# Optimization experiments

Measured on AMD Instinct MI355X. Metric: run time of the kernel, lower is better.

Reference implementation:

```python
import jax, jax.numpy as jnp
import numpy as np

EMBED_DIM = 768
N_HEADS = 12
HEAD_DIM = EMBED_DIM // N_HEADS


def setup_inputs() -> dict:
    key = jax.random.key(0)
    ks = jax.random.split(key, 6)
    bsz, seq = 2, 4096
    hidden_states = jax.random.normal(ks[0], (bsz, seq, EMBED_DIM), dtype=jnp.float32)
    attention_mask = jnp.zeros((bsz, 1, 1, seq), dtype=jnp.float32)
    s = 1.0 / np.sqrt(EMBED_DIM)
    Wq = jax.random.normal(ks[1], (EMBED_DIM, EMBED_DIM), dtype=jnp.float32) * s
    Wk = jax.random.normal(ks[2], (EMBED_DIM, EMBED_DIM), dtype=jnp.float32) * s
    Wv = jax.random.normal(ks[3], (EMBED_DIM, EMBED_DIM), dtype=jnp.float32) * s
    Wo = jax.random.normal(ks[4], (EMBED_DIM, EMBED_DIM), dtype=jnp.float32) * s
    bo = jax.random.normal(ks[5], (EMBED_DIM,), dtype=jnp.float32) * s
    return {"hidden_states": hidden_states, "attention_mask": attention_mask,
            "Wq": Wq, "Wk": Wk, "Wv": Wv, "Wo": Wo, "bo": bo}


def reference(hidden_states, attention_mask, Wq, Wk, Wv, Wo, bo):
    bsz, seq, _ = hidden_states.shape
    scale = 1.0 / np.sqrt(HEAD_DIM)

    def split_heads(x):  # [b, s, e] -> [b, h, s, d]
        return x.reshape(bsz, seq, N_HEADS, HEAD_DIM).transpose(0, 2, 1, 3)

    # nn.Linear applies x @ W.T
    q = split_heads(hidden_states @ Wq.T)
    k = split_heads(hidden_states @ Wk.T)
    v = split_heads(hidden_states @ Wv.T)

    # [b, h, tgt, src] score matrix (faithful to the bmm+softmax+bmm original)
    attn = jnp.einsum('bhqd,bhkd->bhqk', q, k) * scale
    attn = attn + attention_mask  # mask broadcasts [b,1,1,src]
    probs = jax.nn.softmax(attn, axis=-1)
    ctx = jnp.einsum('bhqk,bhkd->bhqd', probs, v)

    concat = ctx.transpose(0, 2, 1, 3).reshape(bsz, seq, EMBED_DIM)
    return concat @ Wo.T + bo
```

## Files before the change

kernel.cpp:

```cpp
#include <hip/hip_runtime.h>
#include <stdint.h>

#define ED   768
#define NH   12
#define HD   64
#define SEQ  4096
#define BSZ  2
#define BHT  (BSZ*NH)
#define MTOT (BSZ*SEQ)

typedef short bf16x8  __attribute__((ext_vector_type(8)));
typedef float f32x4   __attribute__((ext_vector_type(4)));
typedef float f32x16  __attribute__((ext_vector_type(16)));
typedef unsigned int u32x4 __attribute__((ext_vector_type(4)));

#define LOG2E 1.44269504088896340736f
#define C2    (0.125f * LOG2E)

__device__ __forceinline__ unsigned short f2bf(float f) {
    union { float f; uint32_t u; } v; v.f = f;
    uint32_t u = v.u;
    u += 0x7fffu + ((u >> 16) & 1u);
    return (unsigned short)(u >> 16);
}

__device__ __forceinline__ uint32_t cvtpk(float lo, float hi) {
    uint32_t r;
    asm("v_cvt_pk_bf16_f32 %0, %1, %2" : "=v"(r) : "v"(lo), "v"(hi));
    return r;
}

__device__ __forceinline__ void cp16(const unsigned short* g, unsigned short* l) {
    __builtin_amdgcn_global_load_lds(
        (const __attribute__((address_space(1))) unsigned int*)(const void*)g,
        (__attribute__((address_space(3))) unsigned int*)(void*)l,
        16, 0, 0);
}

#define H_CHUNKS  (MTOT * ED / 4)
#define W_CHUNKS  (ED * ED / 4)
#define CVT_TOTAL (H_CHUNKS + 4 * W_CHUNKS)

__global__ __launch_bounds__(256) void convert_bf16(
    const float* __restrict__ H,  const float* __restrict__ Wq,
    const float* __restrict__ Wk, const float* __restrict__ Wv,
    const float* __restrict__ Wo, unsigned short* __restrict__ dst,
    unsigned short* __restrict__ WoB) {
    int i4 = blockIdx.x * 256 + threadIdx.x;
    float4 v;
    ushort4* optr;
    if (i4 < H_CHUNKS) { v = ((const float4*)H)[i4]; optr = (ushort4*)dst + i4; }
    else {
        int j = i4 - H_CHUNKS;
        if (j < 3 * W_CHUNKS) {
            if (j < W_CHUNKS)          v = ((const float4*)Wq)[j];
            else if (j < 2 * W_CHUNKS) v = ((const float4*)Wk)[j - W_CHUNKS];
            else                       v = ((const float4*)Wv)[j - 2 * W_CHUNKS];
            optr = (ushort4*)dst + i4;
        } else {
            v = ((const float4*)Wo)[j - 3 * W_CHUNKS];
            optr = (ushort4*)WoB + (j - 3 * W_CHUNKS);
        }
    }
    ushort4 o;
    o.x = f2bf(v.x); o.y = f2bf(v.y); o.z = f2bf(v.z); o.w = f2bf(v.w);
    *optr = o;
}

__global__ __launch_bounds__(256) void qkv_gemm(
    const unsigned short* __restrict__ Hb,
    const unsigned short* __restrict__ Wb,
    unsigned short* __restrict__ qkv) {
    __shared__ __align__(16) unsigned short Ah[128 * 64];
    __shared__ __align__(16) unsigned short Bh[128 * 64];
    const int t = threadIdx.x, w = t >> 6, lane = t & 63;
    const int quad = lane >> 4, r16 = lane & 15;
    const int wm = w >> 1, wn = w & 1;
    const int m0 = blockIdx.y * 128, n0g = blockIdx.x * 128;
    const int wsel = n0g / ED, n0 = n0g % ED;
    const int lrow = lane >> 3;
    const int lchs = ((lane & 7) ^ (lrow & 7)) * 8;

    f32x4 acc[4][4] = {};
    for (int kt = 0; kt < ED / 64; ++kt) {
        const int k0 = kt * 64;
#pragma unroll
        for (int i = 0; i < 4; ++i) {
            int row = i * 32 + w * 8;
            cp16(&Hb[(size_t)(m0 + row + lrow) * ED + k0 + lchs], &Ah[row * 64]);
            cp16(&Wb[(size_t)(n0g + row + lrow) * ED + k0 + lchs], &Bh[row * 64]);
        }
        __syncthreads();
#pragma unroll
        for (int kk = 0; kk < 2; ++kk) {
            bf16x8 aF[4], bF[4];
#pragma unroll
            for (int mi = 0; mi < 4; ++mi) {
                int R = wm * 64 + mi * 16 + r16;
                aF[mi] = *(const bf16x8*)&Ah[R * 64 + (((kk * 4 + quad) ^ (r16 & 7)) * 8)];
            }
#pragma unroll
            for (int ni = 0; ni < 4; ++ni) {
                int R = wn * 64 + ni * 16 + r16;
                bF[ni] = *(const bf16x8*)&Bh[R * 64 + (((kk * 4 + quad) ^ (r16 & 7)) * 8)];
            }
            if (wsel == 2) {
#pragma unroll
                for (int mi = 0; mi < 4; ++mi)
#pragma unroll
                    for (int ni = 0; ni < 4; ++ni)
                        acc[mi][ni] = __builtin_amdgcn_mfma_f32_16x16x32_bf16(
                            bF[ni], aF[mi], acc[mi][ni], 0, 0, 0);
            } else {
#pragma unroll
                for (int mi = 0; mi < 4; ++mi)
#pragma unroll
                    for (int ni = 0; ni < 4; ++ni)
                        acc[mi][ni] = __builtin_amdgcn_mfma_f32_16x16x32_bf16(
                            aF[mi], bF[ni], acc[mi][ni], 0, 0, 0);
            }
        }
        __syncthreads();
    }
    const size_t WSZ = (size_t)BHT * SEQ * HD;
    if (wsel == 2) {
#pragma unroll
        for (int mi = 0; mi < 4; ++mi)
#pragma unroll
            for (int ni = 0; ni < 4; ++ni)
#pragma unroll
                for (int r = 0; r < 4; ++r) {
                    int m  = m0 + wm * 64 + mi * 16 + r16;
                    int nn = n0 + wn * 64 + ni * 16 + quad * 4 + r;
                    int b = m >> 12, s = m & 4095;
                    int hh = nn >> 6, dd = nn & 63;
                    qkv[2 * WSZ + (((size_t)b * NH + hh) * HD + dd) * SEQ + s] =
                        f2bf(acc[mi][ni][r]);
                }
    } else {
        const float sc = (wsel == 0) ? C2 : 1.0f;
#pragma unroll
        for (int mi = 0; mi < 4; ++mi)
#pragma unroll
            for (int ni = 0; ni < 4; ++ni)
#pragma unroll
                for (int r = 0; r < 4; ++r) {
                    int m = m0 + wm * 64 + mi * 16 + quad * 4 + r;
                    int b = m >> 12, s = m & 4095;
                    int nn = n0 + wn * 64 + ni * 16 + r16;
                    int hh = nn >> 6, dd = nn & 63;
                    size_t off = (((size_t)b * NH + hh) * SEQ + s) * HD + dd;
                    qkv[(size_t)wsel * WSZ + off] = f2bf(acc[mi][ni][r] * sc);
                }
    }
}

__global__ __launch_bounds__(256) void flash_attn(
    const unsigned short* __restrict__ qkv, const float* __restrict__ mask,
    unsigned short* __restrict__ ctx) {
    __shared__ __align__(16) unsigned short Ksm[2][64 * 64];
    __shared__ __align__(16) unsigned short Vtsm[2][64 * 64];
    __shared__ __align__(16) unsigned short Mall[SEQ];
    const int t  = threadIdx.x;
    const int bh = blockIdx.y;
    const int b  = bh / NH;
    const int h  = bh % NH;
    const int qbase = blockIdx.x * 128;
    const size_t WSZ = (size_t)BHT * SEQ * HD;
    const unsigned short* Qp = qkv + (size_t)bh * SEQ * HD;
    const unsigned short* Kp = Qp + WSZ;
    const unsigned short* Vt = qkv + 2 * WSZ + (size_t)bh * HD * SEQ;
    const int w = t >> 6, lane = t & 63, n31 = lane & 31, hi = lane >> 5;
    const int lrow = lane >> 3;
    const int lchs = ((lane & 7) ^ (lrow & 7)) * 8;

    bf16x8 qF[4];
    {
        int qrow = qbase + w * 32 + n31;
#pragma unroll
        for (int kc = 0; kc < 4; ++kc)
            qF[kc] = *(const bf16x8*)&Qp[(size_t)qrow * HD + kc * 16 + hi * 8];
    }
    bf16x8 bOnes = {};
    if (hi == 0) bOnes[0] = (short)0x3F80;
    bf16x8 aOnes;
#pragma unroll
    for (int i = 0; i < 8; ++i) aOnes[i] = (short)0x3F80;

#pragma unroll
    for (int i = 0; i < 4; ++i) {
        float4 mv = ((const float4*)(mask + (size_t)b * SEQ))[i * 256 + t];
        ushort4 o;
        o.x = f2bf(LOG2E * mv.x); o.y = f2bf(LOG2E * mv.y);
        o.z = f2bf(LOG2E * mv.z); o.w = f2bf(LOG2E * mv.w);
        *(ushort4*)&Mall[(i * 256 + t) * 4] = o;
    }

#pragma unroll
    for (int i = 0; i < 2; ++i) {
        int row = w * 16 + i * 8;
        cp16(&Kp[(size_t)(row + lrow) * HD + lchs], &Ksm[0][row * 64]);
        cp16(&Vt[(size_t)(row + lrow) * SEQ + lchs], &Vtsm[0][row * 64]);
    }
    __syncthreads();

    f32x16 oAcc[2] = {};
    f32x16 lAcc = {};
    const int sw = n31 & 7;
    int cur = 0;

    for (int kt = 0; kt < SEQ / 64; ++kt) {
        if (kt + 1 < SEQ / 64) {
#pragma unroll
            for (int i = 0; i < 2; ++i) {
                int row = w * 16 + i * 8;
                cp16(&Kp[(size_t)((kt + 1) * 64 + row + lrow) * HD + lchs],
                     &Ksm[cur ^ 1][row * 64]);
                cp16(&Vt[(size_t)(row + lrow) * SEQ + (kt + 1) * 64 + lchs],
                     &Vtsm[cur ^ 1][row * 64]);
            }
        }

        float p[2][16];
#pragma unroll
        for (int st = 0; st < 2; ++st) {
            bf16x8 am = {};
            {
                unsigned short mv = Mall[kt * 64 + st * 32 + n31];
                am[0] = (hi == 0) ? (short)mv : (short)0;
            }
            f32x16 sA = {};
            sA = __builtin_amdgcn_mfma_f32_32x32x16_bf16(am, bOnes, sA, 0, 0, 0);
            __builtin_amdgcn_s_setprio(1);
#pragma unroll
            for (int kc = 0; kc < 4; ++kc) {
                bf16x8 kF = *(const bf16x8*)
                    &Ksm[cur][(st * 32 + n31) * 64 + (((2 * kc + hi) ^ sw) * 8)];
                sA = __builtin_amdgcn_mfma_f32_32x32x16_bf16(kF, qF[kc], sA, 0, 0, 0);
            }
            __builtin_amdgcn_s_setprio(0);
#pragma unroll
            for (int r = 0; r < 16; ++r) p[st][r] = __builtin_amdgcn_exp2f(sA[r]);
        }

        bf16x8 pF[4];
#pragma unroll
        for (int st = 0; st < 2; ++st) {
            uint32_t pw[8];
#pragma unroll
            for (int i = 0; i < 8; ++i)
                pw[i] = cvtpk(p[st][2 * i], p[st][2 * i + 1]);
#pragma unroll
            for (int half = 0; half < 2; ++half) {
                auto r02 = __builtin_amdgcn_permlane32_swap(
                    pw[half * 4 + 0], pw[half * 4 + 2], false, false);
                auto r13 = __builtin_amdgcn_permlane32_swap(
                    pw[half * 4 + 1], pw[half * 4 + 3], false, false);
                union { u32x4 u; bf16x8 h; } f;
                f.u[0] = r02[0]; f.u[1] = r13[0]; f.u[2] = r02[1]; f.u[3] = r13[1];
                pF[st * 2 + half] = f.h;
            }
        }

        __builtin_amdgcn_s_setprio(1);
#pragma unroll
        for (int kc = 0; kc < 4; ++kc) {
            lAcc = __builtin_amdgcn_mfma_f32_32x32x16_bf16(
                aOnes, pF[kc], lAcc, 0, 0, 0);
#pragma unroll
            for (int dt = 0; dt < 2; ++dt) {
                bf16x8 vF = *(const bf16x8*)
                    &Vtsm[cur][(dt * 32 + n31) * 64 + (((2 * kc + hi) ^ sw) * 8)];
                oAcc[dt] = __builtin_amdgcn_mfma_f32_32x32x16_bf16(vF, pF[kc], oAcc[dt], 0, 0, 0);
            }
        }
        __builtin_amdgcn_s_setprio(0);

        __syncthreads();
        cur ^= 1;
    }
    float inv = 1.0f / lAcc[0];
    int s = qbase + w * 32 + n31;
    unsigned short* obase = &ctx[((size_t)b * SEQ + s) * ED + h * HD];
#pragma unroll
    for (int dt = 0; dt < 2; ++dt)
#pragma unroll
        for (int g = 0; g < 4; ++g) {
            ushort4 o;
            o.x = f2bf(oAcc[dt][4 * g + 0] * inv);
            o.y = f2bf(oAcc[dt][4 * g + 1] * inv);
            o.z = f2bf(oAcc[dt][4 * g + 2] * inv);
            o.w = f2bf(oAcc[dt][4 * g + 3] * inv);
            *(ushort4*)&obase[dt * 32 + hi * 4 + 8 * g] = o;
        }
}

__global__ __launch_bounds__(256) void out_gemm(
    const unsigned short* __restrict__ Ab,
    const unsigned short* __restrict__ Wob,
    const float* __restrict__ bo, float* __restrict__ out) {
    __shared__ __align__(16) unsigned short Ah[128 * 64];
    __shared__ __align__(16) unsigned short Bh[128 * 64];
    const int t = threadIdx.x, w = t >> 6, lane = t & 63;
    const int quad = lane >> 4, r16 = lane & 15;
    const int wm = w >> 1, wn = w & 1;
    const int m0 = blockIdx.y * 128, n0 = blockIdx.x * 128;
    const int lrow = lane >> 3;
    const int lchs = ((lane & 7) ^ (lrow & 7)) * 8;

    f32x4 acc[4][4] = {};
    for (int kt = 0; kt < ED / 64; ++kt) {
        const int k0 = kt * 64;
#pragma unroll
        for (int i = 0; i < 4; ++i) {
            int row = i * 32 + w * 8;
            cp16(&Ab[(size_t)(m0 + row + lrow) * ED + k0 + lchs], &Ah[row * 64]);
            cp16(&Wob[(size_t)(n0 + row + lrow) * ED + k0 + lchs], &Bh[row * 64]);
        }
        __syncthreads();
#pragma unroll
        for (int kk = 0; kk < 2; ++kk) {
            bf16x8 aF[4], bF[4];
#pragma unroll
            for (int mi = 0; mi < 4; ++mi) {
                int R = wm * 64 + mi * 16 + r16;
                aF[mi] = *(const bf16x8*)&Ah[R * 64 + (((kk * 4 + quad) ^ (r16 & 7)) * 8)];
            }
#pragma unroll
            for (int ni = 0; ni < 4; ++ni) {
                int R = wn * 64 + ni * 16 + r16;
                bF[ni] = *(const bf16x8*)&Bh[R * 64 + (((kk * 4 + quad) ^ (r16 & 7)) * 8)];
            }
#pragma unroll
            for (int mi = 0; mi < 4; ++mi)
#pragma unroll
                for (int ni = 0; ni < 4; ++ni)
                    acc[mi][ni] = __builtin_amdgcn_mfma_f32_16x16x32_bf16(
                        aF[mi], bF[ni], acc[mi][ni], 0, 0, 0);
        }
        __syncthreads();
    }
    float bov[4];
#pragma unroll
    for (int ni = 0; ni < 4; ++ni) bov[ni] = bo[n0 + wn * 64 + ni * 16 + r16];
#pragma unroll
    for (int mi = 0; mi < 4; ++mi)
#pragma unroll
        for (int ni = 0; ni < 4; ++ni)
#pragma unroll
            for (int r = 0; r < 4; ++r) {
                int m = m0 + wm * 64 + mi * 16 + quad * 4 + r;
                int n = n0 + wn * 64 + ni * 16 + r16;
                out[(size_t)m * ED + n] = acc[mi][ni][r] + bov[ni];
            }
}

extern "C" void kernel_launch(void* const* d_in, const int* in_sizes, int n_in,
                              void* d_out, int out_size, void* d_ws, size_t ws_size,
                              hipStream_t stream) {
    const float* H    = (const float*)d_in[0];
    const float* mask = (const float*)d_in[1];
    const float* Wq   = (const float*)d_in[2];
    const float* Wk   = (const float*)d_in[3];
    const float* Wv   = (const float*)d_in[4];
    const float* Wo   = (const float*)d_in[5];
    const float* bo   = (const float*)d_in[6];
    unsigned short* ws = (unsigned short*)d_ws;
    const size_t WSZ = (size_t)BHT * SEQ * HD;
    unsigned short* qkv = ws;
    unsigned short* ctx = ws + 3 * WSZ;
    unsigned short* WoB = ctx + (size_t)MTOT * ED;
    float* out = (float*)d_out;
    unsigned short* Hb = (unsigned short*)d_out;
    unsigned short* Wb = Hb + (size_t)MTOT * ED;

    convert_bf16<<<CVT_TOTAL / 256, 256, 0, stream>>>(H, Wq, Wk, Wv, Wo, Hb, WoB);
    qkv_gemm<<<dim3(3 * ED / 128, MTOT / 128), 256, 0, stream>>>(Hb, Wb, qkv);
    flash_attn<<<dim3(SEQ / 128, BHT), 256, 0, stream>>>(qkv, mask, ctx);
    out_gemm<<<dim3(ED / 128, MTOT / 128), 256, 0, stream>>>(ctx, WoB, bo, out);
}
```

Before: 295.1 us.

## Split flash attention over key range into two halves with combine kernel

Templates the attention kernel on a key-range split. With SPLIT=2 each block processes half the keys and writes unnormalized fp32 partial outputs and row sums. A new kernel then adds the halves, normalizes and converts to bf16. The intent is to double the available parallelism and shorten each block's serial loop. The cost is extra fp32 global traffic and an additional launch. The split path is used only when the workspace is large enough.

```diff
diff --git a/kernel.cpp b/kernel.cpp
--- a/kernel.cpp
+++ b/kernel.cpp
@@ -22,6 +22,11 @@
     uint32_t u = v.u;
     u += 0x7fffu + ((u >> 16) & 1u);
     return (unsigned short)(u >> 16);
+}
+
+__device__ __forceinline__ float bf2f(unsigned short h) {
+    union { uint32_t u; float f; } v; v.u = ((uint32_t)h) << 16;
+    return v.f;
 }
 
 __device__ __forceinline__ uint32_t cvtpk(float lo, float hi) {
@@ -155,21 +160,26 @@
     }
 }
 
+template <int SPLIT>
 __global__ __launch_bounds__(256) void flash_attn(
     const unsigned short* __restrict__ qkv, const float* __restrict__ mask,
-    unsigned short* __restrict__ ctx) {
+    unsigned short* __restrict__ ctx, float* __restrict__ Ap0,
+    float* __restrict__ Ap1, float* __restrict__ lp) {
+    constexpr int KRANGE = SEQ / SPLIT;
+    constexpr int NT = KRANGE / 64;
     __shared__ __align__(16) unsigned short Ksm[2][64 * 64];
     __shared__ __align__(16) unsigned short Vtsm[2][64 * 64];
-    __shared__ __align__(16) unsigned short Mall[SEQ];
+    __shared__ __align__(16) unsigned short Mall[KRANGE];
     const int t  = threadIdx.x;
     const int bh = blockIdx.y;
     const int b  = bh / NH;
     const int h  = bh % NH;
+    const int half = (SPLIT == 2) ? blockIdx.z : 0;
     const int qbase = blockIdx.x * 128;
     const size_t WSZ = (size_t)BHT * SEQ * HD;
     const unsigned short* Qp = qkv + (size_t)bh * SEQ * HD;
-    const unsigned short* Kp = Qp + WSZ;
-    const unsigned short* Vt = qkv + 2 * WSZ + (size_t)bh * HD * SEQ;
+    const unsigned short* Kp = Qp + WSZ + (size_t)half * KRANGE * HD;
+    const unsigned short* Vt = qkv + 2 * WSZ + (size_t)bh * HD * SEQ + (size_t)half * KRANGE;
     const int w = t >> 6, lane = t & 63, n31 = lane & 31, hi = lane >> 5;
     const int lrow = lane >> 3;
     const int lchs = ((lane & 7) ^ (lrow & 7)) * 8;
@@ -188,8 +198,8 @@
     for (int i = 0; i < 8; ++i) aOnes[i] = (short)0x3F80;
 
 #pragma unroll
-    for (int i = 0; i < 4; ++i) {
-        float4 mv = ((const float4*)(mask + (size_t)b * SEQ))[i * 256 + t];
+    for (int i = 0; i < KRANGE / 1024; ++i) {
+        float4 mv = ((const float4*)(mask + (size_t)b * SEQ + half * KRANGE))[i * 256 + t];
         ushort4 o;
         o.x = f2bf(LOG2E * mv.x); o.y = f2bf(LOG2E * mv.y);
         o.z = f2bf(LOG2E * mv.z); o.w = f2bf(LOG2E * mv.w);
@@ -209,8 +219,8 @@
     const int sw = n31 & 7;
     int cur = 0;
 
-    for (int kt = 0; kt < SEQ / 64; ++kt) {
-        if (kt + 1 < SEQ / 64) {
+    for (int kt = 0; kt < NT; ++kt) {
+        if (kt + 1 < NT) {
 #pragma unroll
             for (int i = 0; i < 2; ++i) {
                 int row = w * 16 + i * 8;
@@ -251,14 +261,14 @@
             for (int i = 0; i < 8; ++i)
                 pw[i] = cvtpk(p[st][2 * i], p[st][2 * i + 1]);
 #pragma unroll
-            for (int half = 0; half < 2; ++half) {
+            for (int half2 = 0; half2 < 2; ++half2) {
                 auto r02 = __builtin_amdgcn_permlane32_swap(
-                    pw[half * 4 + 0], pw[half * 4 + 2], false, false);
+                    pw[half2 * 4 + 0], pw[half2 * 4 + 2], false, false);
                 auto r13 = __builtin_amdgcn_permlane32_swap(
-                    pw[half * 4 + 1], pw[half * 4 + 3], false, false);
+                    pw[half2 * 4 + 1], pw[half2 * 4 + 3], false, false);
                 union { u32x4 u; bf16x8 h; } f;
                 f.u[0] = r02[0]; f.u[1] = r13[0]; f.u[2] = r02[1]; f.u[3] = r13[1];
-                pF[st * 2 + half] = f.h;
+                pF[st * 2 + half2] = f.h;
             }
         }
 
@@ -279,20 +289,62 @@
         __syncthreads();
         cur ^= 1;
     }
-    float inv = 1.0f / lAcc[0];
+
     int s = qbase + w * 32 + n31;
-    unsigned short* obase = &ctx[((size_t)b * SEQ + s) * ED + h * HD];
-#pragma unroll
-    for (int dt = 0; dt < 2; ++dt)
-#pragma unroll
-        for (int g = 0; g < 4; ++g) {
-            ushort4 o;
-            o.x = f2bf(oAcc[dt][4 * g + 0] * inv);
-            o.y = f2bf(oAcc[dt][4 * g + 1] * inv);
-            o.z = f2bf(oAcc[dt][4 * g + 2] * inv);
-            o.w = f2bf(oAcc[dt][4 * g + 3] * inv);
-            *(ushort4*)&obase[dt * 32 + hi * 4 + 8 * g] = o;
-        }
+    if (SPLIT == 1) {
+        float inv = 1.0f / lAcc[0];
+        unsigned short* obase = &ctx[((size_t)b * SEQ + s) * ED + h * HD];
+#pragma unroll
+        for (int dt = 0; dt < 2; ++dt)
+#pragma unroll
+            for (int g = 0; g < 4; ++g) {
+                ushort4 o;
+                o.x = f2bf(oAcc[dt][4 * g + 0] * inv);
+                o.y = f2bf(oAcc[dt][4 * g + 1] * inv);
+                o.z = f2bf(oAcc[dt][4 * g + 2] * inv);
+                o.w = f2bf(oAcc[dt][4 * g + 3] * inv);
+                *(ushort4*)&obase[dt * 32 + hi * 4 + 8 * g] = o;
+            }
+    } else {
+        float* Ap = half ? Ap1 : Ap0;
+        float* obase = &Ap[((size_t)b * SEQ + s) * ED + h * HD];
+#pragma unroll
+        for (int dt = 0; dt < 2; ++dt)
+#pragma unroll
+            for (int g = 0; g < 4; ++g) {
+                float4 o;
+                o.x = oAcc[dt][4 * g + 0];
+                o.y = oAcc[dt][4 * g + 1];
+                o.z = oAcc[dt][4 * g + 2];
+                o.w = oAcc[dt][4 * g + 3];
+                *(float4*)&obase[dt * 32 + hi * 4 + 8 * g] = o;
+            }
+        if (hi == 0)
+            lp[(size_t)half * BHT * SEQ + (size_t)bh * SEQ + s] = lAcc[0];
+    }
+}
+
+__global__ __launch_bounds__(256) void combine_halves(
+    const float* __restrict__ A0, const float* __restrict__ A1,
+    const float* __restrict__ lp, unsigned short* __restrict__ ctx) {
+    int i8 = blockIdx.x * 256 + threadIdx.x;
+    int e0 = i8 * 8;
+    int m = e0 / ED;
+    int e = e0 - m * ED;
+    int b = m >> 12, s = m & 4095, h = e >> 6;
+    size_t bhs = ((size_t)(b * NH + h)) * SEQ + s;
+    float inv = 1.0f / (lp[bhs] + lp[(size_t)BHT * SEQ + bhs]);
+    float4 a0 = ((const float4*)A0)[i8 * 2];
+    float4 a1 = ((const float4*)A1)[i8 * 2];
+    float4 b0 = ((const float4*)A0)[i8 * 2 + 1];
+    float4 b1 = ((const float4*)A1)[i8 * 2 + 1];
+    ushort4 o0, o1;
+    o0.x = f2bf((a0.x + a1.x) * inv); o0.y = f2bf((a0.y + a1.y) * inv);
+    o0.z = f2bf((a0.z + a1.z) * inv); o0.w = f2bf((a0.w + a1.w) * inv);
+    o1.x = f2bf((b0.x + b1.x) * inv); o1.y = f2bf((b0.y + b1.y) * inv);
+    o1.z = f2bf((b0.z + b1.z) * inv); o1.w = f2bf((b0.w + b1.w) * inv);
+    ((ushort4*)ctx)[i8 * 2]     = o0;
+    ((ushort4*)ctx)[i8 * 2 + 1] = o1;
 }
 
 __global__ __launch_bounds__(256) void out_gemm(
@@ -373,9 +425,21 @@
     float* out = (float*)d_out;
     unsigned short* Hb = (unsigned short*)d_out;
     unsigned short* Wb = Hb + (size_t)MTOT * ED;
+    float* lpart = (float*)(WoB + (size_t)ED * ED);
+    float* A1    = lpart + 2 * (size_t)BHT * SEQ;
+    float* A0    = (float*)d_out;
+    const size_t need = ((size_t)(3 * WSZ + (size_t)MTOT * ED + ED * ED)) * 2
+                      + 2 * (size_t)BHT * SEQ * 4 + (size_t)MTOT * ED * 4;
 
     convert_bf16<<<CVT_TOTAL / 256, 256, 0, stream>>>(H, Wq, Wk, Wv, Wo, Hb, WoB);
     qkv_gemm<<<dim3(3 * ED / 128, MTOT / 128), 256, 0, stream>>>(Hb, Wb, qkv);
-    flash_attn<<<dim3(SEQ / 128, BHT), 256, 0, stream>>>(qkv, mask, ctx);
+    if (ws_size >= need) {
+        flash_attn<2><<<dim3(SEQ / 128, BHT, 2), 256, 0, stream>>>(
+            qkv, mask, ctx, A0, A1, lpart);
+        combine_halves<<<(MTOT * ED / 8) / 256, 256, 0, stream>>>(A0, A1, lpart, ctx);
+    } else {
+        flash_attn<1><<<dim3(SEQ / 128, BHT), 256, 0, stream>>>(
+            qkv, mask, ctx, nullptr, nullptr, nullptr);
+    }
     out_gemm<<<dim3(ED / 128, MTOT / 128), 256, 0, stream>>>(ctx, WoB, bo, out);
 }
```

After: 316.3 us. 1.07x slower.

## Triple-buffer K tiles and split barriers with partial vmcnt waits in flash attention

Applied to the files above, without the earlier changes.

Restructures the flash-attention main loop so K tiles are prefetched two iterations ahead into a three-slot LDS ring while V stays double-buffered. The single end-of-iteration __syncthreads is replaced by an s_waitcnt vmcnt(N) plus s_barrier placed before the PV stage and a bare barrier after it, and the last two iterations are peeled out. The aim is to give global-to-LDS loads more time to land and to stop the barrier from draining all outstanding loads. In exchange it uses more LDS, which can lower occupancy, and it relies on exact hand-counted vmcnt values to be correct.

```diff
diff --git a/kernel.cpp b/kernel.cpp
--- a/kernel.cpp
+++ b/kernel.cpp
@@ -155,11 +155,67 @@
     }
 }
 
+#define QK_SM(KOFF, KT, PF) do {                                               \
+    float p_[2][16];                                                           \
+_Pragma("unroll")                                                              \
+    for (int st = 0; st < 2; ++st) {                                           \
+        bf16x8 am = {};                                                        \
+        { unsigned short mv = Mall[(KT) * 64 + st * 32 + n31];                 \
+          am[0] = (hi == 0) ? (short)mv : (short)0; }                          \
+        f32x16 sA = {};                                                        \
+        sA = __builtin_amdgcn_mfma_f32_32x32x16_bf16(am, bOnes, sA, 0, 0, 0);  \
+        __builtin_amdgcn_s_setprio(1);                                         \
+_Pragma("unroll")                                                              \
+        for (int kc = 0; kc < 4; ++kc) {                                       \
+            bf16x8 kF = *(const bf16x8*)                                       \
+                &Ksm[(KOFF) + (st * 32 + n31) * 64 + (((2 * kc + hi) ^ sw) * 8)]; \
+            sA = __builtin_amdgcn_mfma_f32_32x32x16_bf16(kF, qF[kc], sA, 0, 0, 0); \
+        }                                                                      \
+        __builtin_amdgcn_s_setprio(0);                                         \
+_Pragma("unroll")                                                              \
+        for (int r = 0; r < 16; ++r) p_[st][r] = __builtin_amdgcn_exp2f(sA[r]); \
+    }                                                                          \
+_Pragma("unroll")                                                              \
+    for (int st = 0; st < 2; ++st) {                                           \
+        uint32_t pw[8];                                                        \
+_Pragma("unroll")                                                              \
+        for (int i = 0; i < 8; ++i)                                            \
+            pw[i] = cvtpk(p_[st][2 * i], p_[st][2 * i + 1]);                   \
+_Pragma("unroll")                                                              \
+        for (int hf = 0; hf < 2; ++hf) {                                       \
+            auto r02 = __builtin_amdgcn_permlane32_swap(                       \
+                pw[hf * 4 + 0], pw[hf * 4 + 2], false, false);                 \
+            auto r13 = __builtin_amdgcn_permlane32_swap(                       \
+                pw[hf * 4 + 1], pw[hf * 4 + 3], false, false);                 \
+            union { u32x4 u; bf16x8 h; } f_;                                   \
+            f_.u[0] = r02[0]; f_.u[1] = r13[0]; f_.u[2] = r02[1]; f_.u[3] = r13[1]; \
+            PF[st * 2 + hf] = f_.h;                                            \
+        }                                                                      \
+    }                                                                          \
+} while (0)
+
+#define PV_ACC(VOFF, PF) do {                                                  \
+    __builtin_amdgcn_s_setprio(1);                                             \
+_Pragma("unroll")                                                              \
+    for (int kc = 0; kc < 4; ++kc) {                                           \
+        lAcc = __builtin_amdgcn_mfma_f32_32x32x16_bf16(                        \
+            aOnes, PF[kc], lAcc, 0, 0, 0);                                     \
+_Pragma("unroll")                                                              \
+        for (int dt = 0; dt < 2; ++dt) {                                       \
+            bf16x8 vF = *(const bf16x8*)                                       \
+                &Vtsm[(VOFF) + (dt * 32 + n31) * 64 + (((2 * kc + hi) ^ sw) * 8)]; \
+            oAcc[dt] = __builtin_amdgcn_mfma_f32_32x32x16_bf16(                \
+                vF, PF[kc], oAcc[dt], 0, 0, 0);                                \
+        }                                                                      \
+    }                                                                          \
+    __builtin_amdgcn_s_setprio(0);                                             \
+} while (0)
+
 __global__ __launch_bounds__(256) void flash_attn(
     const unsigned short* __restrict__ qkv, const float* __restrict__ mask,
     unsigned short* __restrict__ ctx) {
-    __shared__ __align__(16) unsigned short Ksm[2][64 * 64];
-    __shared__ __align__(16) unsigned short Vtsm[2][64 * 64];
+    __shared__ __align__(16) unsigned short Ksm[3 * 4096];
+    __shared__ __align__(16) unsigned short Vtsm[2 * 4096];
     __shared__ __align__(16) unsigned short Mall[SEQ];
     const int t  = threadIdx.x;
     const int bh = blockIdx.y;
@@ -196,89 +252,55 @@
         *(ushort4*)&Mall[(i * 256 + t) * 4] = o;
     }
 
-#pragma unroll
-    for (int i = 0; i < 2; ++i) {
-        int row = w * 16 + i * 8;
-        cp16(&Kp[(size_t)(row + lrow) * HD + lchs], &Ksm[0][row * 64]);
-        cp16(&Vt[(size_t)(row + lrow) * SEQ + lchs], &Vtsm[0][row * 64]);
-    }
+    const int row0 = w * 16, row1 = w * 16 + 8;
+
+    cp16(&Kp[(size_t)(row0 + lrow) * HD + lchs],      &Ksm[row0 * 64]);
+    cp16(&Kp[(size_t)(row1 + lrow) * HD + lchs],      &Ksm[row1 * 64]);
+    cp16(&Kp[(size_t)(64 + row0 + lrow) * HD + lchs], &Ksm[4096 + row0 * 64]);
+    cp16(&Kp[(size_t)(64 + row1 + lrow) * HD + lchs], &Ksm[4096 + row1 * 64]);
+    cp16(&Vt[(size_t)(row0 + lrow) * SEQ + lchs],     &Vtsm[row0 * 64]);
+    cp16(&Vt[(size_t)(row1 + lrow) * SEQ + lchs],     &Vtsm[row1 * 64]);
     __syncthreads();
 
     f32x16 oAcc[2] = {};
     f32x16 lAcc = {};
     const int sw = n31 & 7;
-    int cur = 0;
-
-    for (int kt = 0; kt < SEQ / 64; ++kt) {
-        if (kt + 1 < SEQ / 64) {
-#pragma unroll
-            for (int i = 0; i < 2; ++i) {
-                int row = w * 16 + i * 8;
-                cp16(&Kp[(size_t)((kt + 1) * 64 + row + lrow) * HD + lchs],
-                     &Ksm[cur ^ 1][row * 64]);
-                cp16(&Vt[(size_t)(row + lrow) * SEQ + (kt + 1) * 64 + lchs],
-                     &Vtsm[cur ^ 1][row * 64]);
-            }
-        }
-
-        float p[2][16];
-#pragma unroll
-        for (int st = 0; st < 2; ++st) {
-            bf16x8 am = {};
-            {
-                unsigned short mv = Mall[kt * 64 + st * 32 + n31];
-                am[0] = (hi == 0) ? (short)mv : (short)0;
-            }
-            f32x16 sA = {};
-            sA = __builtin_amdgcn_mfma_f32_32x32x16_bf16(am, bOnes, sA, 0, 0, 0);
-            __builtin_amdgcn_s_setprio(1);
-#pragma unroll
-            for (int kc = 0; kc < 4; ++kc) {
-                bf16x8 kF = *(const bf16x8*)
-                    &Ksm[cur][(st * 32 + n31) * 64 + (((2 * kc + hi) ^ sw) * 8)];
-                sA = __builtin_amdgcn_mfma_f32_32x32x16_bf16(kF, qF[kc], sA, 0, 0, 0);
-            }
-            __builtin_amdgcn_s_setprio(0);
-#pragma unroll
-            for (int r = 0; r < 16; ++r) p[st][r] = __builtin_amdgcn_exp2f(sA[r]);
-        }
+    int kCur = 0, kNxt = 4096, kFar = 8192;
+    int vCur = 0;
+
+    for (int kt = 0; kt < 62; ++kt) {
+        cp16(&Kp[(size_t)((kt + 2) * 64 + row0 + lrow) * HD + lchs], &Ksm[kFar + row0 * 64]);
+        cp16(&Kp[(size_t)((kt + 2) * 64 + row1 + lrow) * HD + lchs], &Ksm[kFar + row1 * 64]);
+        cp16(&Vt[(size_t)(row0 + lrow) * SEQ + (kt + 1) * 64 + lchs], &Vtsm[(vCur ^ 4096) + row0 * 64]);
+        cp16(&Vt[(size_t)(row1 + lrow) * SEQ + (kt + 1) * 64 + lchs], &Vtsm[(vCur ^ 4096) + row1 * 64]);
 
         bf16x8 pF[4];
-#pragma unroll
-        for (int st = 0; st < 2; ++st) {
-            uint32_t pw[8];
-#pragma unroll
-            for (int i = 0; i < 8; ++i)
-                pw[i] = cvtpk(p[st][2 * i], p[st][2 * i + 1]);
-#pragma unroll
-            for (int half = 0; half < 2; ++half) {
-                auto r02 = __builtin_amdgcn_permlane32_swap(
-                    pw[half * 4 + 0], pw[half * 4 + 2], false, false);
-                auto r13 = __builtin_amdgcn_permlane32_swap(
-                    pw[half * 4 + 1], pw[half * 4 + 3], false, false);
-                union { u32x4 u; bf16x8 h; } f;
-                f.u[0] = r02[0]; f.u[1] = r13[0]; f.u[2] = r02[1]; f.u[3] = r13[1];
-                pF[st * 2 + half] = f.h;
-            }
-        }
-
-        __builtin_amdgcn_s_setprio(1);
-#pragma unroll
-        for (int kc = 0; kc < 4; ++kc) {
-            lAcc = __builtin_amdgcn_mfma_f32_32x32x16_bf16(
-                aOnes, pF[kc], lAcc, 0, 0, 0);
-#pragma unroll
-            for (int dt = 0; dt < 2; ++dt) {
-                bf16x8 vF = *(const bf16x8*)
-                    &Vtsm[cur][(dt * 32 + n31) * 64 + (((2 * kc + hi) ^ sw) * 8)];
-                oAcc[dt] = __builtin_amdgcn_mfma_f32_32x32x16_bf16(vF, pF[kc], oAcc[dt], 0, 0, 0);
-            }
-        }
-        __builtin_amdgcn_s_setprio(0);
-
-        __syncthreads();
-        cur ^= 1;
-    }
+        QK_SM(kCur, kt, pF);
+        asm volatile("s_waitcnt vmcnt(4)\n\ts_barrier" ::: "memory");
+        PV_ACC(vCur, pF);
+        asm volatile("s_barrier" ::: "memory");
+
+        int tmp = kCur; kCur = kNxt; kNxt = kFar; kFar = tmp;
+        vCur ^= 4096;
+    }
+    {
+        cp16(&Vt[(size_t)(row0 + lrow) * SEQ + 63 * 64 + lchs], &Vtsm[(vCur ^ 4096) + row0 * 64]);
+        cp16(&Vt[(size_t)(row1 + lrow) * SEQ + 63 * 64 + lchs], &Vtsm[(vCur ^ 4096) + row1 * 64]);
+        bf16x8 pF[4];
+        QK_SM(kCur, 62, pF);
+        asm volatile("s_waitcnt vmcnt(2)\n\ts_barrier" ::: "memory");
+        PV_ACC(vCur, pF);
+        asm volatile("s_barrier" ::: "memory");
+        int tmp = kCur; kCur = kNxt; kNxt = kFar; kFar = tmp;
+        vCur ^= 4096;
+    }
+    {
+        bf16x8 pF[4];
+        QK_SM(kCur, 63, pF);
+        asm volatile("s_waitcnt vmcnt(0)\n\ts_barrier" ::: "memory");
+        PV_ACC(vCur, pF);
+    }
+
     float inv = 1.0f / lAcc[0];
     int s = qbase + w * 32 + n31;
     unsigned short* obase = &ctx[((size_t)b * SEQ + s) * ED + h * HD];
```

After: 320.7 us. +8.7%, slower.

## Load V fragments directly from global and split MFMA accumulator chains

Applied to the files above, without the earlier changes.

Drops the LDS staging of the transposed V tile and has each lane read its V fragments straight from global memory (through cache) inside the PV loop. The K tile is still double-buffered in LDS. The QK^T and PV MFMA accumulations are split into two independent chains (even/odd, and first/second halves) that are summed afterwards, shortening dependent MFMA latency chains. This cuts LDS footprint and traffic but puts global-load latency directly in the MFMA loop with no prefetch, and adds extra registers for the duplicated accumulators.

```diff
diff --git a/kernel.cpp b/kernel.cpp
--- a/kernel.cpp
+++ b/kernel.cpp
@@ -158,8 +158,7 @@
 __global__ __launch_bounds__(256) void flash_attn(
     const unsigned short* __restrict__ qkv, const float* __restrict__ mask,
     unsigned short* __restrict__ ctx) {
-    __shared__ __align__(16) unsigned short Ksm[2][64 * 64];
-    __shared__ __align__(16) unsigned short Vtsm[2][64 * 64];
+    __shared__ __align__(16) unsigned short Ksm[2 * 4096];
     __shared__ __align__(16) unsigned short Mall[SEQ];
     const int t  = threadIdx.x;
     const int bh = blockIdx.y;
@@ -196,32 +195,31 @@
         *(ushort4*)&Mall[(i * 256 + t) * 4] = o;
     }
 
-#pragma unroll
-    for (int i = 0; i < 2; ++i) {
-        int row = w * 16 + i * 8;
-        cp16(&Kp[(size_t)(row + lrow) * HD + lchs], &Ksm[0][row * 64]);
-        cp16(&Vt[(size_t)(row + lrow) * SEQ + lchs], &Vtsm[0][row * 64]);
+    const unsigned short* vR0 = Vt + (size_t)n31 * SEQ + hi * 8;
+    const unsigned short* vR1 = Vt + (size_t)(32 + n31) * SEQ + hi * 8;
+
+    {
+        int row0 = w * 16, row1 = w * 16 + 8;
+        cp16(&Kp[(size_t)(row0 + lrow) * HD + lchs], &Ksm[row0 * 64]);
+        cp16(&Kp[(size_t)(row1 + lrow) * HD + lchs], &Ksm[row1 * 64]);
     }
     __syncthreads();
 
-    f32x16 oAcc[2] = {};
+    f32x16 oA[2] = {}, oB[2] = {};
     f32x16 lAcc = {};
+    const f32x16 Z = {};
     const int sw = n31 & 7;
     int cur = 0;
 
     for (int kt = 0; kt < SEQ / 64; ++kt) {
         if (kt + 1 < SEQ / 64) {
-#pragma unroll
-            for (int i = 0; i < 2; ++i) {
-                int row = w * 16 + i * 8;
-                cp16(&Kp[(size_t)((kt + 1) * 64 + row + lrow) * HD + lchs],
-                     &Ksm[cur ^ 1][row * 64]);
-                cp16(&Vt[(size_t)(row + lrow) * SEQ + (kt + 1) * 64 + lchs],
-                     &Vtsm[cur ^ 1][row * 64]);
-            }
-        }
-
-        float p[2][16];
+            int row0 = w * 16, row1 = w * 16 + 8;
+            int koff = (cur ^ 1) << 12;
+            cp16(&Kp[(size_t)((kt + 1) * 64 + row0 + lrow) * HD + lchs], &Ksm[koff + row0 * 64]);
+            cp16(&Kp[(size_t)((kt + 1) * 64 + row1 + lrow) * HD + lchs], &Ksm[koff + row1 * 64]);
+        }
+
+        bf16x8 pF[4];
 #pragma unroll
         for (int st = 0; st < 2; ++st) {
             bf16x8 am = {};
@@ -229,36 +227,35 @@
                 unsigned short mv = Mall[kt * 64 + st * 32 + n31];
                 am[0] = (hi == 0) ? (short)mv : (short)0;
             }
-            f32x16 sA = {};
-            sA = __builtin_amdgcn_mfma_f32_32x32x16_bf16(am, bOnes, sA, 0, 0, 0);
+            bf16x8 kF[4];
+#pragma unroll
+            for (int kc = 0; kc < 4; ++kc)
+                kF[kc] = *(const bf16x8*)
+                    &Ksm[(cur << 12) + (st * 32 + n31) * 64 + (((2 * kc + hi) ^ sw) * 8)];
+            f32x16 sE = __builtin_amdgcn_mfma_f32_32x32x16_bf16(am, bOnes, Z, 0, 0, 0);
             __builtin_amdgcn_s_setprio(1);
-#pragma unroll
-            for (int kc = 0; kc < 4; ++kc) {
-                bf16x8 kF = *(const bf16x8*)
-                    &Ksm[cur][(st * 32 + n31) * 64 + (((2 * kc + hi) ^ sw) * 8)];
-                sA = __builtin_amdgcn_mfma_f32_32x32x16_bf16(kF, qF[kc], sA, 0, 0, 0);
-            }
+            sE = __builtin_amdgcn_mfma_f32_32x32x16_bf16(kF[0], qF[0], sE, 0, 0, 0);
+            f32x16 sO = __builtin_amdgcn_mfma_f32_32x32x16_bf16(kF[1], qF[1], Z, 0, 0, 0);
+            sE = __builtin_amdgcn_mfma_f32_32x32x16_bf16(kF[2], qF[2], sE, 0, 0, 0);
+            sO = __builtin_amdgcn_mfma_f32_32x32x16_bf16(kF[3], qF[3], sO, 0, 0, 0);
             __builtin_amdgcn_s_setprio(0);
-#pragma unroll
-            for (int r = 0; r < 16; ++r) p[st][r] = __builtin_amdgcn_exp2f(sA[r]);
-        }
-
-        bf16x8 pF[4];
-#pragma unroll
-        for (int st = 0; st < 2; ++st) {
+
+            float p_[16];
+#pragma unroll
+            for (int r = 0; r < 16; ++r) p_[r] = __builtin_amdgcn_exp2f(sE[r] + sO[r]);
             uint32_t pw[8];
 #pragma unroll
             for (int i = 0; i < 8; ++i)
-                pw[i] = cvtpk(p[st][2 * i], p[st][2 * i + 1]);
-#pragma unroll
-            for (int half = 0; half < 2; ++half) {
+                pw[i] = cvtpk(p_[2 * i], p_[2 * i + 1]);
+#pragma unroll
+            for (int hf = 0; hf < 2; ++hf) {
                 auto r02 = __builtin_amdgcn_permlane32_swap(
-                    pw[half * 4 + 0], pw[half * 4 + 2], false, false);
+                    pw[hf * 4 + 0], pw[hf * 4 + 2], false, false);
                 auto r13 = __builtin_amdgcn_permlane32_swap(
-                    pw[half * 4 + 1], pw[half * 4 + 3], false, false);
+                    pw[hf * 4 + 1], pw[hf * 4 + 3], false, false);
                 union { u32x4 u; bf16x8 h; } f;
                 f.u[0] = r02[0]; f.u[1] = r13[0]; f.u[2] = r02[1]; f.u[3] = r13[1];
-                pF[st * 2 + half] = f.h;
+                pF[st * 2 + hf] = f.h;
             }
         }
 
@@ -267,11 +264,14 @@
         for (int kc = 0; kc < 4; ++kc) {
             lAcc = __builtin_amdgcn_mfma_f32_32x32x16_bf16(
                 aOnes, pF[kc], lAcc, 0, 0, 0);
-#pragma unroll
-            for (int dt = 0; dt < 2; ++dt) {
-                bf16x8 vF = *(const bf16x8*)
-                    &Vtsm[cur][(dt * 32 + n31) * 64 + (((2 * kc + hi) ^ sw) * 8)];
-                oAcc[dt] = __builtin_amdgcn_mfma_f32_32x32x16_bf16(vF, pF[kc], oAcc[dt], 0, 0, 0);
+            bf16x8 v0 = *(const bf16x8*)&vR0[kt * 64 + kc * 16];
+            bf16x8 v1 = *(const bf16x8*)&vR1[kt * 64 + kc * 16];
+            if (kc < 2) {
+                oA[0] = __builtin_amdgcn_mfma_f32_32x32x16_bf16(v0, pF[kc], oA[0], 0, 0, 0);
+                oA[1] = __builtin_amdgcn_mfma_f32_32x32x16_bf16(v1, pF[kc], oA[1], 0, 0, 0);
+            } else {
+                oB[0] = __builtin_amdgcn_mfma_f32_32x32x16_bf16(v0, pF[kc], oB[0], 0, 0, 0);
+                oB[1] = __builtin_amdgcn_mfma_f32_32x32x16_bf16(v1, pF[kc], oB[1], 0, 0, 0);
             }
         }
         __builtin_amdgcn_s_setprio(0);
@@ -279,20 +279,23 @@
         __syncthreads();
         cur ^= 1;
     }
+
     float inv = 1.0f / lAcc[0];
     int s = qbase + w * 32 + n31;
     unsigned short* obase = &ctx[((size_t)b * SEQ + s) * ED + h * HD];
 #pragma unroll
-    for (int dt = 0; dt < 2; ++dt)
+    for (int dt = 0; dt < 2; ++dt) {
+        f32x16 oSum = oA[dt] + oB[dt];
 #pragma unroll
         for (int g = 0; g < 4; ++g) {
             ushort4 o;
-            o.x = f2bf(oAcc[dt][4 * g + 0] * inv);
-            o.y = f2bf(oAcc[dt][4 * g + 1] * inv);
-            o.z = f2bf(oAcc[dt][4 * g + 2] * inv);
-            o.w = f2bf(oAcc[dt][4 * g + 3] * inv);
+            o.x = f2bf(oSum[4 * g + 0] * inv);
+            o.y = f2bf(oSum[4 * g + 1] * inv);
+            o.z = f2bf(oSum[4 * g + 2] * inv);
+            o.w = f2bf(oSum[4 * g + 3] * inv);
             *(ushort4*)&obase[dt * 32 + hi * 4 + 8 * g] = o;
         }
+    }
 }
 
 __global__ __launch_bounds__(256) void out_gemm(
```

Result: slower. 486.8 us (+65.0%).
